# Optimization experiments

Measured on AMD Instinct MI355X. Metric: run time of the kernel, lower is better.

## Reference

```python
import jax, jax.numpy as jnp
import numpy as np

NUM_NODES = 100000
NUM_RELS = 200
DIM = 128
NUM_EDGES = 600000


def setup_inputs() -> dict:
    key = jax.random.key(0)
    ks = jax.random.split(key, 12)
    xav = lambda k, shp: jax.random.uniform(k, shp, jnp.float32, -1.0, 1.0) * jnp.sqrt(6.0 / (shp[0] + shp[1]))
    return {
        'edge_index': jax.random.randint(ks[0], (2, NUM_EDGES), 0, NUM_NODES),
        'edge_type': jax.random.randint(ks[1], (NUM_EDGES,), 0, NUM_RELS),
        'edge_weight': jax.random.uniform(ks[2], (NUM_EDGES,), jnp.float32),
        'node_emb': xav(ks[3], (NUM_NODES, DIM)),
        'rel_emb': xav(ks[4], (NUM_RELS, DIM)),
        'W0': xav(ks[5], (DIM, DIM)),
        'Wself0': xav(ks[6], (DIM, DIM)),
        'Wrel0': xav(ks[7], (DIM, DIM)),
        'W1': xav(ks[8], (DIM, DIM)),
        'Wself1': xav(ks[9], (DIM, DIM)),
        'Wrel1': xav(ks[10], (DIM, DIM)),
    }


def comp_sub(x_src, r):
    return x_src - r


def compgcn_conv(x, rel, edge_index, edge_type, edge_weight, W, Wself, Wrel):
    src, dst = edge_index[0], edge_index[1]
    # edge-wise gather + composition: [E, D]
    msg = comp_sub(x[src], rel[edge_type])
    msg = msg * edge_weight[:, None]
    # scatter-add aggregation to destination nodes: [N, D]
    agg = jax.ops.segment_sum(msg, dst, num_segments=x.shape[0])
    x_out = agg @ W + x @ Wself
    rel_out = rel @ Wrel
    return x_out, rel_out


def reference(edge_index, edge_type, edge_weight, node_emb, rel_emb,
              W0, Wself0, Wrel0, W1, Wself1, Wrel1):
    # layer 0
    x, rel = compgcn_conv(node_emb, rel_emb, edge_index, edge_type, edge_weight,
                          W0, Wself0, Wrel0)
    # inter-layer nonlinearity (dropout is identity in eval mode)
    x = jax.nn.relu(x)
    rel = jax.nn.relu(rel)
    # layer 1 (last layer: no relu/dropout after)
    x, rel = compgcn_conv(x, rel, edge_index, edge_type, edge_weight,
                          W1, Wself1, Wrel1)
    return x, rel
```

## Files before the change

### kernel.cpp

```cpp
#include <hip/hip_runtime.h>

#define DD 128

typedef __attribute__((ext_vector_type(8))) short bf16x8;
typedef __attribute__((ext_vector_type(4))) float f32x4;

__device__ __forceinline__ float b2f(unsigned short u) {
    return __uint_as_float(((unsigned)u) << 16);
}
__device__ __forceinline__ unsigned short f2b(float f) {
    unsigned u = __float_as_uint(f);
    unsigned r = (u + 0x7FFFu + ((u >> 16) & 1u)) >> 16;
    return (unsigned short)r;
}


__global__ __launch_bounds__(256) void scan1_kernel(const int* __restrict__ cnt,
                                                    int* __restrict__ startv,
                                                    int* __restrict__ bsum, int n) {
    int i = blockIdx.x * 256 + threadIdx.x;
    int v = (i < n) ? cnt[i] : 0;
    int lane = threadIdx.x & 63, wid = threadIdx.x >> 6;
    int incl = v;
#pragma unroll
    for (int o = 1; o < 64; o <<= 1) {
        int t = __shfl_up(incl, o);
        if (lane >= o) incl += t;
    }
    __shared__ int wsum[4];
    __shared__ int wpre[4];
    if (lane == 63) wsum[wid] = incl;
    __syncthreads();
    if (threadIdx.x == 0) {
        int s = 0;
        for (int w2 = 0; w2 < 4; ++w2) { wpre[w2] = s; s += wsum[w2]; }
        bsum[blockIdx.x] = s;
    }
    __syncthreads();
    if (i < n) startv[i] = incl - v + wpre[wid];
}

__global__ __launch_bounds__(512) void scan2_kernel(int* bsum, int nb) {
    int i = threadIdx.x;
    int v = (i < nb) ? bsum[i] : 0;
    int lane = threadIdx.x & 63, wid = threadIdx.x >> 6;
    int incl = v;
#pragma unroll
    for (int o = 1; o < 64; o <<= 1) {
        int t = __shfl_up(incl, o);
        if (lane >= o) incl += t;
    }
    __shared__ int wsum[8];
    __shared__ int wpre[8];
    if (lane == 63) wsum[wid] = incl;
    __syncthreads();
    if (threadIdx.x == 0) {
        int s = 0;
        for (int w2 = 0; w2 < 8; ++w2) { wpre[w2] = s; s += wsum[w2]; }
    }
    __syncthreads();
    if (i < nb) bsum[i] = incl - v + wpre[wid];
}

__global__ __launch_bounds__(256) void scan3_kernel(int* startv, int* cursor,
                                                    const int* __restrict__ bsum,
                                                    int n, int E) {
    int i = blockIdx.x * 256 + threadIdx.x;
    if (i < n) {
        int s = startv[i] + bsum[i >> 8];
        startv[i] = s;
        cursor[i] = s;
    } else if (i == n) {
        startv[n] = E;
    }
}

__global__ __launch_bounds__(256) void fill_kernel(const int* __restrict__ ei,
                                                   const int* __restrict__ ety,
                                                   const float* __restrict__ ew,
                                                   int* cursor,
                                                   uint2* __restrict__ csre, int E) {
    int e0 = blockIdx.x * 512 + threadIdx.x;
    int e1 = e0 + 256;
    if (e0 < E) {
        int dst = ei[E + e0];
        int p = atomicAdd(&cursor[dst], 1);
        uint2 rec;
        rec.x = ((unsigned)ei[e0]) | (((unsigned)ety[e0]) << 20);
        rec.y = __float_as_uint(ew[e0]);
        __builtin_nontemporal_store(*(unsigned long long*)&rec,
                                    (unsigned long long*)&csre[p]);
    }
    if (e1 < E) {
        int dst = ei[E + e1];
        int p = atomicAdd(&cursor[dst], 1);
        uint2 rec;
        rec.x = ((unsigned)ei[e1]) | (((unsigned)ety[e1]) << 20);
        rec.y = __float_as_uint(ew[e1]);
        __builtin_nontemporal_store(*(unsigned long long*)&rec,
                                    (unsigned long long*)&csre[p]);
    }
}


__global__ __launch_bounds__(256) void prep_hist_kernel(
    const float* __restrict__ x0, unsigned short* __restrict__ xb, int bx, int n4x,
    const float* __restrict__ r0, unsigned short* __restrict__ r0b, int br, int n4r,
    const float* __restrict__ W0, const float* __restrict__ Ws0,
    const float* __restrict__ W1, const float* __restrict__ Ws1,
    const float* __restrict__ Wr0, const float* __restrict__ Wr1,
    unsigned short* __restrict__ wt0a, unsigned short* __restrict__ wt0s,
    unsigned short* __restrict__ wt1a, unsigned short* __restrict__ wt1s,
    unsigned short* __restrict__ wtr0, unsigned short* __restrict__ wtr1,
    const int* __restrict__ ei, int* __restrict__ cnt, int E) {
    int bid = blockIdx.x;
    if (bid < bx) {
        int i = bid * 256 + threadIdx.x;
        if (i < n4x) {
            float4 v = ((const float4*)x0)[i];
            ((ushort4*)xb)[i] = make_ushort4(f2b(v.x), f2b(v.y), f2b(v.z), f2b(v.w));
        }
        return;
    }
    bid -= bx;
    if (bid < br) {
        int i = bid * 256 + threadIdx.x;
        if (i < n4r) {
            float4 v = ((const float4*)r0)[i];
            ((ushort4*)r0b)[i] = make_ushort4(f2b(v.x), f2b(v.y), f2b(v.z), f2b(v.w));
        }
        return;
    }
    bid -= br;
    if (bid < 384) {
        int which = bid >> 6;
        int i = (bid & 63) * 256 + threadIdx.x;
        int cc = i >> 7, k = i & 127;
        const float* Wsel = which == 0 ? W0 : which == 1 ? Ws0 : which == 2 ? W1
                          : which == 3 ? Ws1 : which == 4 ? Wr0 : Wr1;
        unsigned short* Osel = which == 0 ? wt0a : which == 1 ? wt0s : which == 2 ? wt1a
                             : which == 3 ? wt1s : which == 4 ? wtr0 : wtr1;
        Osel[i] = f2b(Wsel[k * DD + cc]);
        return;
    }
    bid -= 384;
    int e = bid * 256 + threadIdx.x;
    if (e < E) atomicAdd(&cnt[ei[E + e]], 1);
}


__global__ __launch_bounds__(256) void aggregate_kernel(
    const unsigned short* __restrict__ xb, const unsigned short* __restrict__ relb,
    const int* __restrict__ startv, const uint2* __restrict__ csre,
    unsigned short* __restrict__ aggb, int n) {
    int slot = threadIdx.x >> 4;
    int c = threadIdx.x & 15;
    int n0 = blockIdx.x * 32 + slot;
    int n1 = n0 + 16;
    int i0 = 0, e0 = 0, i1 = 0, e1 = 0;
    if (n0 < n) { i0 = startv[n0]; e0 = startv[n0 + 1]; }
    if (n1 < n) { i1 = startv[n1]; e1 = startv[n1 + 1]; }
    const bf16x8* X = (const bf16x8*)xb;
    const bf16x8* Rl = (const bf16x8*)relb;
    float p0[8], q0[8], p1[8], q1[8];
#pragma unroll
    for (int j = 0; j < 8; ++j) { p0[j] = 0.f; q0[j] = 0.f; p1[j] = 0.f; q1[j] = 0.f; }
    while (i0 < e0 || i1 < e1) {
        bool v00 = i0 < e0, v01 = i0 + 1 < e0;
        bool v10 = i1 < e1, v11 = i1 + 1 < e1;
        uint2 c00 = csre[v00 ? i0 : 0];
        uint2 c01 = csre[v01 ? i0 + 1 : 0];
        uint2 c10 = csre[v10 ? i1 : 0];
        uint2 c11 = csre[v11 ? i1 + 1 : 0];
        float w00 = v00 ? __uint_as_float(c00.y) : 0.f;
        float w01 = v01 ? __uint_as_float(c01.y) : 0.f;
        float w10 = v10 ? __uint_as_float(c10.y) : 0.f;
        float w11 = v11 ? __uint_as_float(c11.y) : 0.f;
        bf16x8 x00 = X[(size_t)(c00.x & 0xFFFFFu) * 16 + c];
        bf16x8 x01 = X[(size_t)(c01.x & 0xFFFFFu) * 16 + c];
        bf16x8 x10 = X[(size_t)(c10.x & 0xFFFFFu) * 16 + c];
        bf16x8 x11 = X[(size_t)(c11.x & 0xFFFFFu) * 16 + c];
        bf16x8 r00 = Rl[(c00.x >> 20) * 16 + c];
        bf16x8 r01 = Rl[(c01.x >> 20) * 16 + c];
        bf16x8 r10 = Rl[(c10.x >> 20) * 16 + c];
        bf16x8 r11 = Rl[(c11.x >> 20) * 16 + c];
#pragma unroll
        for (int j = 0; j < 8; ++j) {
            p0[j] += (b2f((unsigned short)x00[j]) - b2f((unsigned short)r00[j])) * w00;
            q0[j] += (b2f((unsigned short)x01[j]) - b2f((unsigned short)r01[j])) * w01;
            p1[j] += (b2f((unsigned short)x10[j]) - b2f((unsigned short)r10[j])) * w10;
            q1[j] += (b2f((unsigned short)x11[j]) - b2f((unsigned short)r11[j])) * w11;
        }
        i0 = min(i0 + 2, e0);
        i1 = min(i1 + 2, e1);
    }
    if (n0 < n) {
        bf16x8 ov;
#pragma unroll
        for (int j = 0; j < 8; ++j) ov[j] = (short)f2b(p0[j] + q0[j]);
        ((bf16x8*)aggb)[(size_t)n0 * 16 + c] = ov;
    }
    if (n1 < n) {
        bf16x8 ov;
#pragma unroll
        for (int j = 0; j < 8; ++j) ov[j] = (short)f2b(p1[j] + q1[j]);
        ((bf16x8*)aggb)[(size_t)n1 * 16 + c] = ov;
    }
}


__global__ __launch_bounds__(512, 4) void mfma_dual_gemm_kernel(
    const unsigned short* __restrict__ A, const unsigned short* __restrict__ X,
    const unsigned short* __restrict__ WtA, const unsigned short* __restrict__ WtX,
    float* __restrict__ outf, unsigned short* __restrict__ outb,
    int nrows, int relu,
    const unsigned short* __restrict__ relsrc, const unsigned short* __restrict__ WtR,
    float* __restrict__ reloutf, unsigned short* __restrict__ reloutb,
    int R, int gbl) {
    __shared__ unsigned short sW[2][DD * DD];
    bool isrel = (int)blockIdx.x >= gbl;
    const unsigned short* srcA = isrel ? WtR : WtA;
    for (int i = threadIdx.x; i < 2048; i += 512) {
        int row = i >> 4, slot = i & 15;
        int so = (slot ^ (row & 15)) * 8;
        *(float4*)&sW[0][row * DD + so] = ((const float4*)srcA)[i];
        *(float4*)&sW[1][row * DD + so] = ((const float4*)WtX)[i];
    }
    __syncthreads();
    int w = threadIdx.x >> 6, l = threadIdx.x & 63;
    int lr = l & 15, lk = l >> 4;

    f32x4 acc[8];
#pragma unroll
    for (int ct = 0; ct < 8; ++ct) acc[ct] = (f32x4){0.f, 0.f, 0.f, 0.f};

    if (!isrel) {
        int row = blockIdx.x * 128 + w * 16 + lr;
        bool v = row < nrows;
#pragma unroll
        for (int kb = 0; kb < 4; ++kb) {
            int koff = kb * 32 + lk * 8;
            bf16x8 a = {}, x = {};
            if (v) {
                a = *(const bf16x8*)(A + (size_t)row * DD + koff);
                x = *(const bf16x8*)(X + (size_t)row * DD + koff);
            }
#pragma unroll
            for (int ct = 0; ct < 8; ++ct) {
                int wrow = ct * 16 + lr;
                int slot = kb * 4 + lk;
                int so = (slot ^ (wrow & 15)) * 8;
                bf16x8 bw = *(const bf16x8*)&sW[0][wrow * DD + so];
                bf16x8 bs = *(const bf16x8*)&sW[1][wrow * DD + so];
                acc[ct] = __builtin_amdgcn_mfma_f32_16x16x32_bf16(bw, a, acc[ct], 0, 0, 0);
                acc[ct] = __builtin_amdgcn_mfma_f32_16x16x32_bf16(bs, x, acc[ct], 0, 0, 0);
            }
        }
        if (v) {
#pragma unroll
            for (int ct = 0; ct < 8; ++ct) {
                f32x4 vv = acc[ct];
                if (relu) {
                    vv[0] = fmaxf(vv[0], 0.f); vv[1] = fmaxf(vv[1], 0.f);
                    vv[2] = fmaxf(vv[2], 0.f); vv[3] = fmaxf(vv[3], 0.f);
                }
                int cb = ct * 16 + lk * 4;
                if (outf) *(f32x4*)(outf + (size_t)row * DD + cb) = vv;
                if (outb) {
                    *(ushort4*)(outb + (size_t)row * DD + cb) =
                        make_ushort4(f2b(vv[0]), f2b(vv[1]), f2b(vv[2]), f2b(vv[3]));
                }
            }
        }
    } else {
        int row = ((int)blockIdx.x - gbl) * 128 + w * 16 + lr;
        bool v = row < R;
#pragma unroll
        for (int kb = 0; kb < 4; ++kb) {
            int koff = kb * 32 + lk * 8;
            bf16x8 a = {};
            if (v) a = *(const bf16x8*)(relsrc + (size_t)row * DD + koff);
#pragma unroll
            for (int ct = 0; ct < 8; ++ct) {
                int wrow = ct * 16 + lr;
                int slot = kb * 4 + lk;
                int so = (slot ^ (wrow & 15)) * 8;
                bf16x8 bw = *(const bf16x8*)&sW[0][wrow * DD + so];
                acc[ct] = __builtin_amdgcn_mfma_f32_16x16x32_bf16(bw, a, acc[ct], 0, 0, 0);
            }
        }
        if (v) {
#pragma unroll
            for (int ct = 0; ct < 8; ++ct) {
                f32x4 vv = acc[ct];
                if (relu) {
                    vv[0] = fmaxf(vv[0], 0.f); vv[1] = fmaxf(vv[1], 0.f);
                    vv[2] = fmaxf(vv[2], 0.f); vv[3] = fmaxf(vv[3], 0.f);
                }
                int cb = ct * 16 + lk * 4;
                if (reloutf) *(f32x4*)(reloutf + (size_t)row * DD + cb) = vv;
                if (reloutb) {
                    *(ushort4*)(reloutb + (size_t)row * DD + cb) =
                        make_ushort4(f2b(vv[0]), f2b(vv[1]), f2b(vv[2]), f2b(vv[3]));
                }
            }
        }
    }
}


extern "C" void kernel_launch(void* const* d_in, const int* in_sizes, int n_in,
                              void* d_out, int out_size, void* d_ws, size_t ws_size,
                              hipStream_t stream) {
    const int*   ei  = (const int*)d_in[0];
    const int*   ety = (const int*)d_in[1];
    const float* ew  = (const float*)d_in[2];
    const float* x0  = (const float*)d_in[3];
    const float* r0  = (const float*)d_in[4];
    const float* W0  = (const float*)d_in[5];
    const float* Ws0 = (const float*)d_in[6];
    const float* Wr0 = (const float*)d_in[7];
    const float* W1  = (const float*)d_in[8];
    const float* Ws1 = (const float*)d_in[9];
    const float* Wr1 = (const float*)d_in[10];

    const int E = in_sizes[1];
    const int N = in_sizes[3] / DD;
    const int R = in_sizes[4] / DD;

    float* out_x = (float*)d_out;
    float* out_r = out_x + (size_t)N * DD;

    char* w = (char*)d_ws;
    size_t off = 0;
    auto alloc = [&](size_t bytes) {
        void* p = w + off;
        off += (bytes + 255) & ~(size_t)255;
        return p;
    };
    unsigned short* aggb  = (unsigned short*)alloc((size_t)N * DD * 2);
    unsigned short* xb    = (unsigned short*)alloc((size_t)N * DD * 2);
    unsigned short* r0b   = (unsigned short*)alloc((size_t)R * DD * 2);
    unsigned short* rel1b = (unsigned short*)alloc((size_t)R * DD * 2);
    unsigned short* wt0a  = (unsigned short*)alloc((size_t)DD * DD * 2);
    unsigned short* wt0s  = (unsigned short*)alloc((size_t)DD * DD * 2);
    unsigned short* wt1a  = (unsigned short*)alloc((size_t)DD * DD * 2);
    unsigned short* wt1s  = (unsigned short*)alloc((size_t)DD * DD * 2);
    unsigned short* wtr0  = (unsigned short*)alloc((size_t)DD * DD * 2);
    unsigned short* wtr1  = (unsigned short*)alloc((size_t)DD * DD * 2);
    int*   startv = (int*)alloc((size_t)(N + 1) * 4);
    int*   cursor = (int*)alloc((size_t)N * 4);
    int*   bsum   = (int*)alloc(512 * 4);
    uint2* csre   = (uint2*)alloc((size_t)E * 8);
    (void)ws_size; (void)n_in; (void)out_size;

    int ebl = (E + 255) / 256;
    int nb  = (N + 255) / 256;
    int n4x = N * 32, n4r = R * 32;
    int bx = (n4x + 255) / 256, br = (n4r + 255) / 256;

    int* cnt = cursor;
    hipMemsetAsync(cnt, 0, (size_t)N * 4, stream);
    prep_hist_kernel<<<bx + br + 384 + ebl, 256, 0, stream>>>(
        x0, xb, bx, n4x, r0, r0b, br, n4r,
        W0, Ws0, W1, Ws1, Wr0, Wr1,
        wt0a, wt0s, wt1a, wt1s, wtr0, wtr1, ei, cnt, E);
    scan1_kernel<<<nb, 256, 0, stream>>>(cnt, startv, bsum, N);
    scan2_kernel<<<1, 512, 0, stream>>>(bsum, nb);
    scan3_kernel<<<(N + 1 + 255) / 256, 256, 0, stream>>>(startv, cursor, bsum, N, E);
    fill_kernel<<<(E + 511) / 512, 256, 0, stream>>>(ei, ety, ew, cursor, csre, E);

    int abl = (N + 31) / 32;
    int gbl = (N + 127) / 128;
    int rblk = (R + 127) / 128;

    aggregate_kernel<<<abl, 256, 0, stream>>>(xb, r0b, startv, csre, aggb, N);
    mfma_dual_gemm_kernel<<<gbl + rblk, 512, 0, stream>>>(
        aggb, xb, wt0a, wt0s, nullptr, xb, N, 1,
        r0b, wtr0, nullptr, rel1b, R, gbl);

    aggregate_kernel<<<abl, 256, 0, stream>>>(xb, rel1b, startv, csre, aggb, N);
    mfma_dual_gemm_kernel<<<gbl + rblk, 512, 0, stream>>>(
        aggb, xb, wt1a, wt1s, out_x, nullptr, N, 0,
        rel1b, wtr1, out_r, nullptr, R, gbl);
}
```

Before: 208.6 us.

## Privatize histogram and fill cursors into 8 partitioned copies

Degree counting and CSR fill now write into 8 privatized counter/cursor arrays, indexed by block id mod 8, instead of one shared array. The scan sums the 8 copies per node and hands out per-partition cursor offsets, and the arrays reuse the aggb scratch buffer. A small zero kernel replaces the memset. The aim is to spread atomics over more addresses and cut contention. The cost is more memory traffic in the scans, plus a zero kernel that must cover the right size (2N int4 covers 8N ints for the counters and cursors).

Result: no change. 208.8 us (+0.1%).

```diff
diff --git a/kernel.cpp b/kernel.cpp
--- a/kernel.cpp
+++ b/kernel.cpp
@@ -15,11 +15,21 @@
 }
 
 
-__global__ __launch_bounds__(256) void scan1_kernel(const int* __restrict__ cnt,
+__global__ __launch_bounds__(256) void zero_kernel(int4* __restrict__ p, int n4) {
+    int i = blockIdx.x * 256 + threadIdx.x;
+    if (i < n4) p[i] = make_int4(0, 0, 0, 0);
+}
+
+
+__global__ __launch_bounds__(256) void scan1_kernel(const int* __restrict__ cnt8,
                                                     int* __restrict__ startv,
                                                     int* __restrict__ bsum, int n) {
     int i = blockIdx.x * 256 + threadIdx.x;
-    int v = (i < n) ? cnt[i] : 0;
+    int v = 0;
+    if (i < n) {
+#pragma unroll
+        for (int p = 0; p < 8; ++p) v += cnt8[p * n + i];
+    }
     int lane = threadIdx.x & 63, wid = threadIdx.x >> 6;
     int incl = v;
 #pragma unroll
@@ -62,14 +72,21 @@
     if (i < nb) bsum[i] = incl - v + wpre[wid];
 }
 
-__global__ __launch_bounds__(256) void scan3_kernel(int* startv, int* cursor,
+__global__ __launch_bounds__(256) void scan3_kernel(int* startv,
+                                                    const int* __restrict__ cnt8,
+                                                    int* __restrict__ cursor8,
                                                     const int* __restrict__ bsum,
                                                     int n, int E) {
     int i = blockIdx.x * 256 + threadIdx.x;
     if (i < n) {
         int s = startv[i] + bsum[i >> 8];
         startv[i] = s;
-        cursor[i] = s;
+        int run = s;
+#pragma unroll
+        for (int p = 0; p < 8; ++p) {
+            cursor8[p * n + i] = run;
+            run += cnt8[p * n + i];
+        }
     } else if (i == n) {
         startv[n] = E;
     }
@@ -78,28 +95,19 @@
 __global__ __launch_bounds__(256) void fill_kernel(const int* __restrict__ ei,
                                                    const int* __restrict__ ety,
                                                    const float* __restrict__ ew,
-                                                   int* cursor,
-                                                   uint2* __restrict__ csre, int E) {
-    int e0 = blockIdx.x * 512 + threadIdx.x;
-    int e1 = e0 + 256;
-    if (e0 < E) {
-        int dst = ei[E + e0];
-        int p = atomicAdd(&cursor[dst], 1);
-        uint2 rec;
-        rec.x = ((unsigned)ei[e0]) | (((unsigned)ety[e0]) << 20);
-        rec.y = __float_as_uint(ew[e0]);
-        __builtin_nontemporal_store(*(unsigned long long*)&rec,
-                                    (unsigned long long*)&csre[p]);
-    }
-    if (e1 < E) {
-        int dst = ei[E + e1];
-        int p = atomicAdd(&cursor[dst], 1);
-        uint2 rec;
-        rec.x = ((unsigned)ei[e1]) | (((unsigned)ety[e1]) << 20);
-        rec.y = __float_as_uint(ew[e1]);
-        __builtin_nontemporal_store(*(unsigned long long*)&rec,
-                                    (unsigned long long*)&csre[p]);
-    }
+                                                   int* cursor8,
+                                                   uint2* __restrict__ csre,
+                                                   int E, int n) {
+    int e = blockIdx.x * 256 + threadIdx.x;
+    if (e >= E) return;
+    int p = blockIdx.x & 7;
+    int dst = ei[E + e];
+    int pos = atomicAdd(&cursor8[p * n + dst], 1);
+    uint2 rec;
+    rec.x = ((unsigned)ei[e]) | (((unsigned)ety[e]) << 20);
+    rec.y = __float_as_uint(ew[e]);
+    __builtin_nontemporal_store(*(unsigned long long*)&rec,
+                                (unsigned long long*)&csre[pos]);
 }
 
 
@@ -112,7 +120,7 @@
     unsigned short* __restrict__ wt0a, unsigned short* __restrict__ wt0s,
     unsigned short* __restrict__ wt1a, unsigned short* __restrict__ wt1s,
     unsigned short* __restrict__ wtr0, unsigned short* __restrict__ wtr1,
-    const int* __restrict__ ei, int* __restrict__ cnt, int E) {
+    const int* __restrict__ ei, int* __restrict__ cnt8, int E, int n) {
     int bid = blockIdx.x;
     if (bid < bx) {
         int i = bid * 256 + threadIdx.x;
@@ -145,7 +153,10 @@
     }
     bid -= 384;
     int e = bid * 256 + threadIdx.x;
-    if (e < E) atomicAdd(&cnt[ei[E + e]], 1);
+    if (e < E) {
+        int p = bid & 7;
+        atomicAdd(&cnt8[p * n + ei[E + e]], 1);
+    }
 }
 
 
@@ -349,26 +360,29 @@
     unsigned short* wtr0  = (unsigned short*)alloc((size_t)DD * DD * 2);
     unsigned short* wtr1  = (unsigned short*)alloc((size_t)DD * DD * 2);
     int*   startv = (int*)alloc((size_t)(N + 1) * 4);
-    int*   cursor = (int*)alloc((size_t)N * 4);
     int*   bsum   = (int*)alloc(512 * 4);
     uint2* csre   = (uint2*)alloc((size_t)E * 8);
     (void)ws_size; (void)n_in; (void)out_size;
+
+    int* cnt8    = (int*)aggb;
+    int* cursor8 = cnt8 + (size_t)8 * N;
 
     int ebl = (E + 255) / 256;
     int nb  = (N + 255) / 256;
     int n4x = N * 32, n4r = R * 32;
     int bx = (n4x + 255) / 256, br = (n4r + 255) / 256;
 
-    int* cnt = cursor;
-    hipMemsetAsync(cnt, 0, (size_t)N * 4, stream);
+    zero_kernel<<<(2 * N + 255) / 256, 256, 0, stream>>>((int4*)cnt8, 2 * N);
+
     prep_hist_kernel<<<bx + br + 384 + ebl, 256, 0, stream>>>(
         x0, xb, bx, n4x, r0, r0b, br, n4r,
         W0, Ws0, W1, Ws1, Wr0, Wr1,
-        wt0a, wt0s, wt1a, wt1s, wtr0, wtr1, ei, cnt, E);
-    scan1_kernel<<<nb, 256, 0, stream>>>(cnt, startv, bsum, N);
+        wt0a, wt0s, wt1a, wt1s, wtr0, wtr1, ei, cnt8, E, N);
+    scan1_kernel<<<nb, 256, 0, stream>>>(cnt8, startv, bsum, N);
     scan2_kernel<<<1, 512, 0, stream>>>(bsum, nb);
-    scan3_kernel<<<(N + 1 + 255) / 256, 256, 0, stream>>>(startv, cursor, bsum, N, E);
-    fill_kernel<<<(E + 511) / 512, 256, 0, stream>>>(ei, ety, ew, cursor, csre, E);
+    scan3_kernel<<<(N + 1 + 255) / 256, 256, 0, stream>>>(startv, cnt8, cursor8,
+                                                          bsum, N, E);
+    fill_kernel<<<ebl, 256, 0, stream>>>(ei, ety, ew, cursor8, csre, E, N);
 
     int abl = (N + 31) / 32;
     int gbl = (N + 127) / 128;
```
